# Optimization experiments

Hardware: AMD Instinct MI355X
Metric: run time of the kernel (lower is better)

## Reference

```python
import jax, jax.numpy as jnp
import numpy as np

B, NEG = 4, 33          # queries, candidates per query
N, R = 10000, 256       # entities, relation types (even; R//2 direct)
D, L = 64, 6            # hidden dim, conv layers
E, ER = 200000, 80000   # entity edges, edges per relation graph (hh/ht/th/tt)
F = 2 * D
EPS = 1e-5


def _ln(x, s, b):
    m = jnp.mean(x, -1, keepdims=True)
    v = jnp.mean((x - m) ** 2, -1, keepdims=True)
    return (x - m) * jax.lax.rsqrt(v + EPS) * s + b


def _conv(x, boundary, relation, src, dst, etype, p):
    # GeneralizedRelationalConv (dependent=False, project_relations=True):
    # distmult message, sum aggregate + boundary self-loop, update=relu(LN(Linear([x,agg])))
    p1w, p1b, p2w, p2b, lw, lb, lns, lnb = p
    rel = jax.nn.relu(relation @ p1w + p1b) @ p2w + p2b     # relation projection MLP
    msg = x[:, src, :] * rel[:, etype, :]                   # [B, Eg, D] gathered messages
    agg = jnp.zeros_like(boundary).at[:, dst, :].add(msg) + boundary
    out = jnp.concatenate([x, agg], -1) @ lw + lb
    return jax.nn.relu(_ln(out, lns, lnb))


def _entity_bf(rel_reps, h0, r0, src, dst, etype, params):
    # NBFNet Bellman-Ford over the entity graph, query-conditioned boundary
    q = rel_reps[jnp.arange(B), r0]                         # [B, D]
    boundary = jnp.zeros((B, N, D), q.dtype).at[jnp.arange(B), h0].add(q)
    x = boundary
    for i in range(L):
        x = _conv(x, boundary, rel_reps, src, dst, etype,
                  tuple(t[i] for t in params)) + x          # short_cut residual
    nq = jnp.broadcast_to(q[:, None, :], (B, N, D))
    return jnp.concatenate([x, nq], -1)                     # [B, N, 2D]


def _forward(floats, ints):
    (e1p1w, e1p1b, e1p2w, e1p2b, e1lw, e1lb, e1lns, e1lnb,
     e2p1w, e2p1b, e2p2w, e2p2b, e2lw, e2lb, e2lns, e2lnb,
     e2m1w, e2m1b, e2m2w, e2m2b,
     rp1w, rp1b, rp2w, rp2b, rlw, rlb, rlns, rlnb, nmw, nmb) = floats
    edge_src, edge_dst, edge_type, rel_src, rel_dst, rel_etype, batch = ints
    h0 = batch[:, 0, 0]
    t_idx = batch[:, :, 1]
    r0 = batch[:, 0, 2]
    e1p = (e1p1w, e1p1b, e1p2w, e1p2b, e1lw, e1lb, e1lns, e1lnb)
    # ---- RelNet over the 4 relation graphs (nodes=relations, edge types=entities) ----
    node_reps = jnp.ones((B, N, D), e1p1w.dtype)
    q = jnp.ones((B, D), e1p1w.dtype)
    boundary = jnp.zeros((B, R, D), q.dtype).at[jnp.arange(B), r0].add(q)
    x = boundary
    for i in range(L):
        h = sum(_conv(x, boundary, node_reps, rel_src[g], rel_dst[g], rel_etype[g],
                      (rp1w[g, i], rp1b[g, i], rp2w[g, i], rp2b[g, i],
                       rlw[g, i], rlb[g, i], rlns[g, i], rlnb[g, i]))
                for g in range(4))
        x = h + x                                           # short_cut
        if i == 0:
            # entity_model_1 refreshes the per-entity (relation-graph edge type) reps
            feat = _entity_bf(x, h0, r0, edge_src, edge_dst, edge_type, e1p)
            node_reps = feat @ nmw + nmb                    # [B, N, D]
    rel_reps = x                                            # [B, R, D]
    # ---- EntityNet 2: score candidates ----
    e2p = (e2p1w, e2p1b, e2p2w, e2p2b, e2lw, e2lb, e2lns, e2lnb)
    feat2 = _entity_bf(rel_reps, h0, r0, edge_src, edge_dst, edge_type, e2p)
    g = jnp.take_along_axis(feat2, jnp.broadcast_to(t_idx[:, :, None], (B, NEG, F)), axis=1)
    score = (jax.nn.relu(g @ e2m1w + e2m1b) @ e2m2w + e2m2b)[..., 0]
    return score                                            # [B, NEG]


def setup_inputs():
    key = jax.random.key(0)
    ks = iter(jax.random.split(key, 64))
    def w(shape, std=0.08):
        return jax.random.normal(next(ks), shape, jnp.float32) * std
    inp = {}
    inp["edge_src"] = jax.random.randint(next(ks), (E,), 0, N, jnp.int32)
    inp["edge_dst"] = jax.random.randint(next(ks), (E,), 0, N, jnp.int32)
    inp["edge_type"] = jax.random.randint(next(ks), (E,), 0, R, jnp.int32)
    inp["rel_src"] = jax.random.randint(next(ks), (4, ER), 0, R, jnp.int32)
    inp["rel_dst"] = jax.random.randint(next(ks), (4, ER), 0, R, jnp.int32)
    inp["rel_etype"] = jax.random.randint(next(ks), (4, ER), 0, N, jnp.int32)
    h = jax.random.randint(next(ks), (B, 1), 0, N, jnp.int32)
    t = jax.random.randint(next(ks), (B, NEG), 0, N, jnp.int32)
    r = jax.random.randint(next(ks), (B, 1), 0, R // 2, jnp.int32)
    inp["batch"] = jnp.stack([jnp.broadcast_to(h, (B, NEG)), t,
                              jnp.broadcast_to(r, (B, NEG))], -1)
    for pre in ("e1", "e2"):
        inp[pre + "p1w"] = w((L, D, D)); inp[pre + "p1b"] = jnp.zeros((L, D))
        inp[pre + "p2w"] = w((L, D, D)); inp[pre + "p2b"] = jnp.zeros((L, D))
        inp[pre + "lw"] = w((L, F, D));  inp[pre + "lb"] = jnp.zeros((L, D))
        inp[pre + "lns"] = jnp.ones((L, D)); inp[pre + "lnb"] = jnp.zeros((L, D))
    inp["e2m1w"] = w((F, F)); inp["e2m1b"] = jnp.zeros((F,))
    inp["e2m2w"] = w((F, 1)); inp["e2m2b"] = jnp.zeros((1,))
    inp["rp1w"] = w((4, L, D, D)); inp["rp1b"] = jnp.zeros((4, L, D))
    inp["rp2w"] = w((4, L, D, D)); inp["rp2b"] = jnp.zeros((4, L, D))
    inp["rlw"] = w((4, L, F, D));  inp["rlb"] = jnp.zeros((4, L, D))
    inp["rlns"] = jnp.ones((4, L, D)); inp["rlnb"] = jnp.zeros((4, L, D))
    inp["nmw"] = w((F, D)); inp["nmb"] = jnp.zeros((D,))
    return inp


def reference(e1p1w, e1p1b, e1p2w, e1p2b, e1lw, e1lb, e1lns, e1lnb,
              e2p1w, e2p1b, e2p2w, e2p2b, e2lw, e2lb, e2lns, e2lnb,
              e2m1w, e2m1b, e2m2w, e2m2b,
              rp1w, rp1b, rp2w, rp2b, rlw, rlb, rlns, rlnb, nmw, nmb,
              edge_src, edge_dst, edge_type, rel_src, rel_dst, rel_etype, batch):
    floats = (e1p1w, e1p1b, e1p2w, e1p2b, e1lw, e1lb, e1lns, e1lnb,
              e2p1w, e2p1b, e2p2w, e2p2b, e2lw, e2lb, e2lns, e2lnb,
              e2m1w, e2m1b, e2m2w, e2m2b,
              rp1w, rp1b, rp2w, rp2b, rlw, rlb, rlns, rlnb, nmw, nmb)
    ints = (edge_src, edge_dst, edge_type, rel_src, rel_dst, rel_etype, batch)
    return _forward(floats, ints)
```

## Files before the change

### kernel.cpp

```cpp
#include <hip/hip_runtime.h>

constexpr int kB   = 4;
constexpr int kNEG = 33;
constexpr int kN   = 10000;
constexpr int kR   = 256;
constexpr int kD   = 64;
constexpr int kL   = 6;
constexpr int kE   = 200000;
constexpr int kER  = 80000;

typedef const float* fp;
typedef __attribute__((ext_vector_type(8))) short bf16x8;
typedef __attribute__((ext_vector_type(4))) float f32x4;

__device__ __forceinline__ float rdlane(float v, int l) {
  return __uint_as_float(__builtin_amdgcn_readlane(__float_as_uint(v), l));
}
__device__ __forceinline__ float wave_sum64(float v) {
  #pragma unroll
  for (int o = 32; o > 0; o >>= 1) v += __shfl_xor(v, o, 64);
  return v;
}
__device__ __forceinline__ short f2bf(float x) {
  unsigned u = __float_as_uint(x);
  unsigned r = (u + 0x7fffu + ((u >> 16) & 1u)) >> 16;
  return (short)r;
}
__device__ __forceinline__ float bf2f_u(unsigned short s) {
  return __uint_as_float(((unsigned)s) << 16);
}
__device__ __forceinline__ float bf2f(short s) { return bf2f_u((unsigned short)s); }

__global__ void k_fill(float* __restrict__ p, float v, int n) {
  int i = blockIdx.x * blockDim.x + threadIdx.x;
  int stride = gridDim.x * blockDim.x;
  for (; i < n; i += stride) p[i] = v;
}
__global__ void k_zero_i(int* __restrict__ p, int n) {
  int i = blockIdx.x * blockDim.x + threadIdx.x;
  int stride = gridDim.x * blockDim.x;
  for (; i < n; i += stride) p[i] = 0;
}
__global__ void k_add_row(float* __restrict__ dst, const int* __restrict__ batch) {
  int tid = threadIdx.x;
  int b = tid >> 6, d = tid & 63;
  int row = batch[b * kNEG * 3 + 2];
  dst[((size_t)b * kR + row) * 64 + d] += 1.0f;
}
__global__ void k_get_q(float* __restrict__ q, const float* __restrict__ relx,
                        const int* __restrict__ batch) {
  int tid = threadIdx.x;
  int b = tid >> 6, d = tid & 63;
  int r0 = batch[b * kNEG * 3 + 2];
  q[b * 64 + d] = relx[((size_t)b * kR + r0) * 64 + d];
}

__global__ void k_hist(const int* __restrict__ dst, int ne, int* __restrict__ cnt) {
  int i = blockIdx.x * blockDim.x + threadIdx.x;
  if (i < ne) atomicAdd(&cnt[dst[i]], 1);
}
__global__ void k_fill_csr(const int* __restrict__ src, const int* __restrict__ dst,
                           const int* __restrict__ et, int ne,
                           int* __restrict__ cursor, int2* __restrict__ out) {
  int i = blockIdx.x * blockDim.x + threadIdx.x;
  if (i < ne) {
    int p = atomicAdd(&cursor[dst[i]], 1);
    out[p] = make_int2(src[i], et[i]);
  }
}
__global__ void k_hist_rel_lds(const int* __restrict__ rel_dst, int* __restrict__ cnt) {
  int g = blockIdx.y;
  __shared__ int lc[256];
  lc[threadIdx.x] = 0;
  __syncthreads();
  int lo = blockIdx.x * 8000, hi = min(lo + 8000, kER);
  for (int e = lo + threadIdx.x; e < hi; e += 256)
    atomicAdd(&lc[rel_dst[(size_t)g * kER + e]], 1);
  __syncthreads();
  int c = lc[threadIdx.x];
  if (c) atomicAdd(&cnt[g * 256 + threadIdx.x], c);
}
__global__ void k_fill_rel_lds(const int* __restrict__ src, const int* __restrict__ dst,
                               const int* __restrict__ et,
                               int* __restrict__ cursor, int2* __restrict__ out) {
  int g = blockIdx.y;
  __shared__ int lc[256];
  lc[threadIdx.x] = 0;
  __syncthreads();
  int lo = blockIdx.x * 8000, hi = min(lo + 8000, kER);
  const int* db = dst + (size_t)g * kER;
  for (int e = lo + threadIdx.x; e < hi; e += 256)
    atomicAdd(&lc[db[e]], 1);
  __syncthreads();
  int c = lc[threadIdx.x];
  __syncthreads();
  lc[threadIdx.x] = c ? atomicAdd(&cursor[g * 257 + threadIdx.x], c) : 0;
  __syncthreads();
  for (int e = lo + threadIdx.x; e < hi; e += 256) {
    int bin = db[e];
    int p = atomicAdd(&lc[bin], 1);
    out[(size_t)g * kER + p] = make_int2(src[(size_t)g * kER + e], et[(size_t)g * kER + e]);
  }
}
__global__ void k_scan_multi(const int* __restrict__ cnt, int* __restrict__ start,
                             int* __restrict__ cursor, int n, int cstride, int sstride) {
  const int* c = cnt + (size_t)blockIdx.x * cstride;
  int* st = start + (size_t)blockIdx.x * sstride;
  int* cu = cursor + (size_t)blockIdx.x * sstride;
  __shared__ int part[256];
  int t = threadIdx.x;
  int chunk = (n + 255) / 256;
  int lo = t * chunk, hi = min(lo + chunk, n);
  int s = 0;
  for (int i = lo; i < hi; ++i) s += c[i];
  part[t] = s;
  __syncthreads();
  if (t == 0) { int run = 0; for (int i = 0; i < 256; ++i) { int v = part[i]; part[i] = run; run += v; } }
  __syncthreads();
  int run = part[t];
  for (int i = lo; i < hi; ++i) { st[i] = run; cu[i] = run; run += c[i]; }
  if (t == 255) st[n] = run;
}

__global__ void k_packw(const float* __restrict__ w1, const float* __restrict__ w2,
                        short* __restrict__ w1h, short* __restrict__ w1l,
                        short* __restrict__ w2h, short* __restrict__ w2l) {
  int pg = blockIdx.x;
  for (int i = threadIdx.x; i < 4096; i += 256) {
    int t = i & 7, lane = (i >> 3) & 63, nt = (i >> 9) & 3, ks = i >> 11;
    int mr = lane & 15, kg = lane >> 4;
    int src = pg * 4096 + (ks * 32 + kg * 8 + t) * 64 + nt * 16 + mr;
    int dst = pg * 4096 + i;
    float v1 = w1[src]; short h1 = f2bf(v1);
    w1h[dst] = h1; w1l[dst] = f2bf(v1 - bf2f(h1));
    float v2 = w2[src]; short h2 = f2bf(v2);
    w2h[dst] = h2; w2l[dst] = f2bf(v2 - bf2f(h2));
  }
}

__global__ void __launch_bounds__(256) k_mlp_mfma(
    const float* __restrict__ in, const short* __restrict__ w1h, const short* __restrict__ w1l,
    const float* __restrict__ b1, const short* __restrict__ w2h, const short* __restrict__ w2l,
    const float* __restrict__ b2, int layer, unsigned short* __restrict__ out) {
  int g = blockIdx.y;
  int pg = g * kL + layer;
  int w = threadIdx.x >> 6, lane = threadIdx.x & 63;
  int mrow = lane & 15, kgrp = lane >> 4;
  int r0 = blockIdx.x * 64 + w * 16;
  __shared__ float hbuf[4][16][68];
  const float* xp = in + (size_t)(r0 + mrow) * 64 + kgrp * 8;
  bf16x8 a1h[2], a1l[2];
  #pragma unroll
  for (int ks = 0; ks < 2; ++ks) {
    #pragma unroll
    for (int t = 0; t < 8; ++t) {
      float v = xp[ks * 32 + t];
      short h = f2bf(v); a1h[ks][t] = h; a1l[ks][t] = f2bf(v - bf2f(h));
    }
  }
  const bf16x8* B1h = (const bf16x8*)(w1h + (size_t)pg * 4096);
  const bf16x8* B1l = (const bf16x8*)(w1l + (size_t)pg * 4096);
  #pragma unroll
  for (int nt = 0; nt < 4; ++nt) {
    f32x4 c = {0.f, 0.f, 0.f, 0.f};
    #pragma unroll
    for (int ks = 0; ks < 2; ++ks) {
      bf16x8 bh = B1h[(ks * 4 + nt) * 64 + lane];
      bf16x8 bl = B1l[(ks * 4 + nt) * 64 + lane];
      c = __builtin_amdgcn_mfma_f32_16x16x32_bf16(a1h[ks], bh, c, 0, 0, 0);
      c = __builtin_amdgcn_mfma_f32_16x16x32_bf16(a1h[ks], bl, c, 0, 0, 0);
      c = __builtin_amdgcn_mfma_f32_16x16x32_bf16(a1l[ks], bh, c, 0, 0, 0);
    }
    int col = nt * 16 + mrow;
    float bv = b1[pg * 64 + col];
    #pragma unroll
    for (int rg = 0; rg < 4; ++rg)
      hbuf[w][kgrp * 4 + rg][col] = fmaxf(c[rg] + bv, 0.f);
  }
  __syncthreads();
  bf16x8 a2h[2], a2l[2];
  #pragma unroll
  for (int ks = 0; ks < 2; ++ks) {
    #pragma unroll
    for (int t = 0; t < 8; ++t) {
      float v = hbuf[w][mrow][ks * 32 + kgrp * 8 + t];
      short h = f2bf(v); a2h[ks][t] = h; a2l[ks][t] = f2bf(v - bf2f(h));
    }
  }
  const bf16x8* B2h = (const bf16x8*)(w2h + (size_t)pg * 4096);
  const bf16x8* B2l = (const bf16x8*)(w2l + (size_t)pg * 4096);
  unsigned short* ob = out + (size_t)g * kB * kN * 64;
  #pragma unroll
  for (int nt = 0; nt < 4; ++nt) {
    f32x4 c = {0.f, 0.f, 0.f, 0.f};
    #pragma unroll
    for (int ks = 0; ks < 2; ++ks) {
      bf16x8 bh = B2h[(ks * 4 + nt) * 64 + lane];
      bf16x8 bl = B2l[(ks * 4 + nt) * 64 + lane];
      c = __builtin_amdgcn_mfma_f32_16x16x32_bf16(a2h[ks], bh, c, 0, 0, 0);
      c = __builtin_amdgcn_mfma_f32_16x16x32_bf16(a2h[ks], bl, c, 0, 0, 0);
      c = __builtin_amdgcn_mfma_f32_16x16x32_bf16(a2l[ks], bh, c, 0, 0, 0);
    }
    int col = nt * 16 + mrow;
    float bv = b2[pg * 64 + col];
    #pragma unroll
    for (int rg = 0; rg < 4; ++rg) {
      int grow = r0 + kgrp * 4 + rg;
      int bb = grow / kN;
      int nn = grow - bb * kN;
      ob[(size_t)nn * 256 + col * 4 + bb] = (unsigned short)f2bf(c[rg] + bv);
    }
  }
}

__global__ void __launch_bounds__(256) k_mlp_rel6(
    const float* __restrict__ in, fp p1w, fp p1b, fp p2w, fp p2b,
    unsigned short* __restrict__ out) {
  int j = blockIdx.y;
  int row = blockIdx.x * 4 + (threadIdx.x >> 6);
  int lane = threadIdx.x & 63;
  fp W1 = p1w + (size_t)j * 4096;
  fp W2 = p2w + (size_t)j * 4096;
  float xv = in[(size_t)row * 64 + lane];
  float a = p1b[j * 64 + lane];
  float wbuf[8];
  #pragma unroll
  for (int kk = 0; kk < 64; kk += 8) {
    #pragma unroll
    for (int u = 0; u < 8; ++u) wbuf[u] = W1[(kk + u) * 64 + lane];
    #pragma unroll
    for (int u = 0; u < 8; ++u) a = fmaf(rdlane(xv, kk + u), wbuf[u], a);
  }
  a = fmaxf(a, 0.f);
  float c = p2b[j * 64 + lane];
  #pragma unroll
  for (int kk = 0; kk < 64; kk += 8) {
    #pragma unroll
    for (int u = 0; u < 8; ++u) wbuf[u] = W2[(kk + u) * 64 + lane];
    #pragma unroll
    for (int u = 0; u < 8; ++u) c = fmaf(rdlane(a, kk + u), wbuf[u], c);
  }
  int b = row >> 8, r = row & 255;
  out[((size_t)j * kR + r) * 256 + lane * 4 + b] = (unsigned short)f2bf(c);
}

__global__ void k_gate0(fp p1w, fp p1b, fp p2w, fp p2b, float* __restrict__ gate0) {
  int g = threadIdx.x >> 6, lane = threadIdx.x & 63;
  int pg = g * kL;
  float a = p1b[pg * 64 + lane];
  #pragma unroll
  for (int k = 0; k < 64; ++k) a += p1w[(size_t)pg * 4096 + k * 64 + lane];
  a = fmaxf(a, 0.f);
  float c = p2b[pg * 64 + lane];
  #pragma unroll
  for (int k = 0; k < 64; ++k)
    c = fmaf(rdlane(a, k), p2w[(size_t)pg * 4096 + k * 64 + lane], c);
  gate0[g * 64 + lane] = c;
}
__global__ void k_rel_agg0(const int* __restrict__ rel_start, const int2* __restrict__ rel_edges,
                           const int* __restrict__ batch, const float* __restrict__ gate0,
                           float* __restrict__ agg) {
  int wid = (blockIdx.x * blockDim.x + threadIdx.x) >> 6;
  int lane = threadIdx.x & 63;
  int g = wid >> 10, rem = wid & 1023, b = rem >> 8, r = rem & 255;
  int r0 = batch[b * kNEG * 3 + 2];
  const int* start = rel_start + g * 257;
  const int2* edges = rel_edges + (size_t)g * kER;
  int s0 = start[r], s1 = start[r + 1];
  int cnt = 0;
  for (int base = s0; base < s1; base += 64) {
    int e = base + lane;
    bool m = false;
    if (e < s1) m = (edges[e].x == r0);
    cnt += (int)__popcll(__ballot(m));
  }
  agg[(size_t)wid * 64 + lane] = gate0[g * 64 + lane] * (float)cnt + ((r == r0) ? 1.f : 0.f);
}

__global__ void __launch_bounds__(256) k_gather_rel_all(
    const float* __restrict__ rxi, const unsigned short* __restrict__ gateN,
    const int* __restrict__ rel_start, const int2* __restrict__ rel_edges,
    const int* __restrict__ batch, float* __restrict__ agg) {
  int i = blockIdx.x;
  int g = i & 3, r = i >> 2;
  const unsigned short* gate = gateN + (size_t)g * kB * kN * 64;
  const int* start = rel_start + g * 257;
  const int2* edges = rel_edges + (size_t)g * kER;
  int w = threadIdx.x >> 6, lane = threadIdx.x & 63;
  int s0 = start[r], s1 = start[r + 1];
  int len = s1 - s0;
  int per = (len + 3) >> 2;
  int e0 = s0 + w * per, e1 = min(e0 + per, s1);
  float a0 = 0.f, a1 = 0.f, a2 = 0.f, a3 = 0.f;
  int2 se;
  if (e0 < e1) se = edges[e0];
  for (int e = e0; e < e1; ++e) {
    int2 cur = se;
    if (e + 1 < e1) se = edges[e + 1];
    float4 xv4 = *((const float4*)(rxi + (size_t)cur.x * 256) + lane);
    ushort4 gv4 = *((const ushort4*)(gate + (size_t)cur.y * 256) + lane);
    a0 = fmaf(xv4.x, bf2f_u(gv4.x), a0);
    a1 = fmaf(xv4.y, bf2f_u(gv4.y), a1);
    a2 = fmaf(xv4.z, bf2f_u(gv4.z), a2);
    a3 = fmaf(xv4.w, bf2f_u(gv4.w), a3);
  }
  __shared__ float red[4][4][64];
  red[w][0][lane] = a0; red[w][1][lane] = a1; red[w][2][lane] = a2; red[w][3][lane] = a3;
  __syncthreads();
  float a = red[0][w][lane] + red[1][w][lane] + red[2][w][lane] + red[3][w][lane];
  int r0b = batch[w * kNEG * 3 + 2];
  if (r == r0b) a += 1.0f;
  agg[(((size_t)g * kB + w) * kR + r) * 64 + lane] = a;
}

__global__ void __launch_bounds__(256) k_conv_rel3(
    const float* __restrict__ rel_x, float* __restrict__ agg,
    fp rlw, fp rlb, fp rlns, fp rlnb, int layer) {
  int g = blockIdx.y;
  int pg = g * kL + layer;
  int wave = threadIdx.x >> 6, lane = threadIdx.x & 63;
  int row0 = blockIdx.x * 16 + wave * 4;
  const float* xp = rel_x + (size_t)row0 * 64 + lane;
  float* ap = agg + ((size_t)g * 1024 + row0) * 64 + lane;
  float x0 = xp[0], x1 = xp[64], x2 = xp[128], x3 = xp[192];
  float g0 = ap[0], g1 = ap[64], g2 = ap[128], g3 = ap[192];
  fp w1 = rlw + (size_t)pg * 8192;
  float bv = rlb[pg * 64 + lane];
  float o0 = bv, o1 = bv, o2 = bv, o3 = bv;
  float wbuf[8];
  #pragma unroll
  for (int kk = 0; kk < 128; kk += 8) {
    #pragma unroll
    for (int u = 0; u < 8; ++u) wbuf[u] = w1[(kk + u) * 64 + lane];
    #pragma unroll
    for (int u = 0; u < 8; ++u) {
      int k = kk + u; float w = wbuf[u];
      if (k < 64) {
        o0 = fmaf(rdlane(x0, k), w, o0); o1 = fmaf(rdlane(x1, k), w, o1);
        o2 = fmaf(rdlane(x2, k), w, o2); o3 = fmaf(rdlane(x3, k), w, o3);
      } else {
        o0 = fmaf(rdlane(g0, k - 64), w, o0); o1 = fmaf(rdlane(g1, k - 64), w, o1);
        o2 = fmaf(rdlane(g2, k - 64), w, o2); o3 = fmaf(rdlane(g3, k - 64), w, o3);
      }
    }
  }
  float s = rlns[pg * 64 + lane], t = rlnb[pg * 64 + lane];
  { float m = wave_sum64(o0) * (1.f/64.f); float c = o0 - m;
    float v = wave_sum64(c*c) * (1.f/64.f);
    ap[0] = fmaxf(c * rsqrtf(v + 1e-5f) * s + t, 0.f); }
  { float m = wave_sum64(o1) * (1.f/64.f); float c = o1 - m;
    float v = wave_sum64(c*c) * (1.f/64.f);
    ap[64] = fmaxf(c * rsqrtf(v + 1e-5f) * s + t, 0.f); }
  { float m = wave_sum64(o2) * (1.f/64.f); float c = o2 - m;
    float v = wave_sum64(c*c) * (1.f/64.f);
    ap[128] = fmaxf(c * rsqrtf(v + 1e-5f) * s + t, 0.f); }
  { float m = wave_sum64(o3) * (1.f/64.f); float c = o3 - m;
    float v = wave_sum64(c*c) * (1.f/64.f);
    ap[192] = fmaxf(c * rsqrtf(v + 1e-5f) * s + t, 0.f); }
}

__global__ void k_sum_rel(float* __restrict__ rel_x, float* __restrict__ rxi,
                          const float* __restrict__ y) {
  int i = blockIdx.x * blockDim.x + threadIdx.x;
  float v = rel_x[i] + y[i] + y[65536 + i] + y[131072 + i] + y[196608 + i];
  rel_x[i] = v;
  int d = i & 63, row = i >> 6;
  int b = row >> 8, r = row & 255;
  rxi[(size_t)r * 256 + d * 4 + b] = v;
}

template<bool FIRST>
__global__ void __launch_bounds__(256) k_ent_layer2(
    const float* __restrict__ xcur, float* __restrict__ xnext,
    const unsigned short* __restrict__ xbf_cur, unsigned short* __restrict__ xbf_next,
    const unsigned short* __restrict__ gateL,
    const int* __restrict__ start, const int2* __restrict__ edges,
    const float* __restrict__ q, const int* __restrict__ batch,
    fp lw, fp lb, fp lns, fp lnb) {
  int n = (blockIdx.x * blockDim.x + threadIdx.x) >> 6;
  if (n >= kN) return;
  int lane = threadIdx.x & 63;
  int h0[4]; float qv[4];
  #pragma unroll
  for (int b = 0; b < 4; ++b) { h0[b] = batch[b * kNEG * 3]; qv[b] = q[b * 64 + lane]; }
  float a0 = 0.f, a1 = 0.f, a2 = 0.f, a3 = 0.f;
  int s0 = start[n], s1 = start[n + 1];
  int2 se;
  if (s0 < s1) se = edges[s0];
  for (int e = s0; e < s1; ++e) {
    int2 cur = se;
    if (e + 1 < s1) se = edges[e + 1];
    ushort4 gv4 = *((const ushort4*)(gateL + (size_t)cur.y * 256) + lane);
    if (FIRST) {
      if (cur.x == h0[0]) a0 = fmaf(qv[0], bf2f_u(gv4.x), a0);
      if (cur.x == h0[1]) a1 = fmaf(qv[1], bf2f_u(gv4.y), a1);
      if (cur.x == h0[2]) a2 = fmaf(qv[2], bf2f_u(gv4.z), a2);
      if (cur.x == h0[3]) a3 = fmaf(qv[3], bf2f_u(gv4.w), a3);
    } else {
      ushort4 xv4 = *((const ushort4*)(xbf_cur + (size_t)cur.x * 256) + lane);
      a0 = fmaf(bf2f_u(xv4.x), bf2f_u(gv4.x), a0);
      a1 = fmaf(bf2f_u(xv4.y), bf2f_u(gv4.y), a1);
      a2 = fmaf(bf2f_u(xv4.z), bf2f_u(gv4.z), a2);
      a3 = fmaf(bf2f_u(xv4.w), bf2f_u(gv4.w), a3);
    }
  }
  if (n == h0[0]) a0 += qv[0];
  if (n == h0[1]) a1 += qv[1];
  if (n == h0[2]) a2 += qv[2];
  if (n == h0[3]) a3 += qv[3];
  float x0, x1, x2, x3;
  if (FIRST) {
    x0 = (n == h0[0]) ? qv[0] : 0.f; x1 = (n == h0[1]) ? qv[1] : 0.f;
    x2 = (n == h0[2]) ? qv[2] : 0.f; x3 = (n == h0[3]) ? qv[3] : 0.f;
  } else {
    const float* xp = xcur + (size_t)n * 64 + lane;
    x0 = xp[0]; x1 = xp[640000]; x2 = xp[1280000]; x3 = xp[1920000];
  }
  float bv = lb[lane];
  float o0 = bv, o1 = bv, o2 = bv, o3 = bv;
  float wbuf[8];
  #pragma unroll
  for (int kk = 0; kk < 128; kk += 8) {
    #pragma unroll
    for (int u = 0; u < 8; ++u) wbuf[u] = lw[(kk + u) * 64 + lane];
    #pragma unroll
    for (int u = 0; u < 8; ++u) {
      int k = kk + u; float w = wbuf[u];
      if (k < 64) {
        o0 = fmaf(rdlane(x0, k), w, o0); o1 = fmaf(rdlane(x1, k), w, o1);
        o2 = fmaf(rdlane(x2, k), w, o2); o3 = fmaf(rdlane(x3, k), w, o3);
      } else {
        o0 = fmaf(rdlane(a0, k - 64), w, o0); o1 = fmaf(rdlane(a1, k - 64), w, o1);
        o2 = fmaf(rdlane(a2, k - 64), w, o2); o3 = fmaf(rdlane(a3, k - 64), w, o3);
      }
    }
  }
  float s = lns[lane], t = lnb[lane];
  float* yp = xnext + (size_t)n * 64 + lane;
  float y0, y1, y2, y3;
  { float m = wave_sum64(o0) * (1.f/64.f); float c = o0 - m;
    float v = wave_sum64(c*c) * (1.f/64.f);
    y0 = x0 + fmaxf(c * rsqrtf(v + 1e-5f) * s + t, 0.f); yp[0] = y0; }
  { float m = wave_sum64(o1) * (1.f/64.f); float c = o1 - m;
    float v = wave_sum64(c*c) * (1.f/64.f);
    y1 = x1 + fmaxf(c * rsqrtf(v + 1e-5f) * s + t, 0.f); yp[640000] = y1; }
  { float m = wave_sum64(o2) * (1.f/64.f); float c = o2 - m;
    float v = wave_sum64(c*c) * (1.f/64.f);
    y2 = x2 + fmaxf(c * rsqrtf(v + 1e-5f) * s + t, 0.f); yp[1280000] = y2; }
  { float m = wave_sum64(o3) * (1.f/64.f); float c = o3 - m;
    float v = wave_sum64(c*c) * (1.f/64.f);
    y3 = x3 + fmaxf(c * rsqrtf(v + 1e-5f) * s + t, 0.f); yp[1920000] = y3; }
  ushort4 m4;
  m4.x = (unsigned short)f2bf(y0); m4.y = (unsigned short)f2bf(y1);
  m4.z = (unsigned short)f2bf(y2); m4.w = (unsigned short)f2bf(y3);
  *((ushort4*)(xbf_next + (size_t)n * 256) + lane) = m4;
}

__global__ void __launch_bounds__(256) k_nodeup4(
    const float* __restrict__ x, const float* __restrict__ q,
    fp nmw, fp nmb, float* __restrict__ out) {
  int wid = (blockIdx.x * blockDim.x + threadIdx.x) >> 6;
  int lane = threadIdx.x & 63;
  int r0 = wid * 4;
  if (r0 >= kB * kN) return;
  int b = r0 / kN;
  const float* ip = x + (size_t)r0 * 64 + lane;
  float x0 = ip[0], x1 = ip[64], x2 = ip[128], x3 = ip[192];
  float qv = q[b * 64 + lane];
  float bv = nmb[lane];
  float c0 = bv, c1 = bv, c2 = bv, c3 = bv;
  float wbuf[4];
  #pragma unroll
  for (int kk = 0; kk < 64; kk += 4) {
    #pragma unroll
    for (int u = 0; u < 4; ++u) wbuf[u] = nmw[(kk + u) * 64 + lane];
    #pragma unroll
    for (int u = 0; u < 4; ++u) {
      int k = kk + u; float w = wbuf[u];
      c0 = fmaf(rdlane(x0, k), w, c0); c1 = fmaf(rdlane(x1, k), w, c1);
      c2 = fmaf(rdlane(x2, k), w, c2); c3 = fmaf(rdlane(x3, k), w, c3);
    }
  }
  float qa = 0.f;
  #pragma unroll
  for (int k = 0; k < 64; ++k)
    qa = fmaf(rdlane(qv, k), nmw[(64 + k) * 64 + lane], qa);
  float* op = out + (size_t)r0 * 64 + lane;
  op[0] = c0 + qa; op[64] = c1 + qa; op[128] = c2 + qa; op[192] = c3 + qa;
}

__global__ void k_score(const float* __restrict__ entx, const float* __restrict__ q,
                        const int* __restrict__ batch,
                        fp m1w, fp m1b, fp m2w, fp m2b,
                        float* __restrict__ out) {
  int b = blockIdx.x / kNEG, n = blockIdx.x % kNEG;
  int t = batch[(b * kNEG + n) * 3 + 1];
  int j = threadIdx.x;
  __shared__ float gv[128];
  __shared__ float red[2];
  gv[j] = (j < 64) ? entx[((size_t)b * kN + t) * 64 + j] : q[b * 64 + (j - 64)];
  __syncthreads();
  float acc = m1b[j];
  #pragma unroll 16
  for (int k = 0; k < 128; ++k)
    acc = fmaf(gv[k], m1w[k * 128 + j], acc);
  float h = fmaxf(acc, 0.f) * m2w[j];
  h = wave_sum64(h);
  if ((j & 63) == 0) red[j >> 6] = h;
  __syncthreads();
  if (j == 0) out[b * kNEG + n] = red[0] + red[1] + m2b[0];
}

extern "C" void kernel_launch(void* const* d_in, const int* in_sizes, int n_in,
                              void* d_out, int out_size, void* d_ws, size_t ws_size,
                              hipStream_t stream) {
  const int* edge_src  = (const int*)d_in[0];
  const int* edge_dst  = (const int*)d_in[1];
  const int* edge_type = (const int*)d_in[2];
  const int* rel_src   = (const int*)d_in[3];
  const int* rel_dst   = (const int*)d_in[4];
  const int* rel_etype = (const int*)d_in[5];
  const int* batch     = (const int*)d_in[6];
  fp e1p1w = (fp)d_in[7],  e1p1b = (fp)d_in[8],  e1p2w = (fp)d_in[9],  e1p2b = (fp)d_in[10];
  fp e1lw  = (fp)d_in[11], e1lb  = (fp)d_in[12], e1lns = (fp)d_in[13], e1lnb = (fp)d_in[14];
  fp e2p1w = (fp)d_in[15], e2p1b = (fp)d_in[16], e2p2w = (fp)d_in[17], e2p2b = (fp)d_in[18];
  fp e2lw  = (fp)d_in[19], e2lb  = (fp)d_in[20], e2lns = (fp)d_in[21], e2lnb = (fp)d_in[22];
  fp e2m1w = (fp)d_in[23], e2m1b = (fp)d_in[24], e2m2w = (fp)d_in[25], e2m2b = (fp)d_in[26];
  fp rp1w  = (fp)d_in[27], rp1b  = (fp)d_in[28], rp2w  = (fp)d_in[29], rp2b  = (fp)d_in[30];
  fp rlw   = (fp)d_in[31], rlb   = (fp)d_in[32], rlns  = (fp)d_in[33], rlnb  = (fp)d_in[34];
  fp nmw   = (fp)d_in[35], nmb   = (fp)d_in[36];

  float* ws = (float*)d_ws;
  float* rel_x     = ws;
  float* q         = rel_x + 65536;
  float* gate0     = q + 256;
  float* rxi       = gate0 + 256;
  float* rel_agg   = rxi + 65536;
  float* node_reps = rel_agg + 262144;
  float* ent_xa    = node_reps + 2560000;
  float* ent_xb    = ent_xa + 2560000;
  unsigned short* gateR6 = (unsigned short*)(ent_xb + 2560000);
  unsigned short* gateN  = gateR6 + 393216;
  unsigned short* ent_ba = gateN + 10240000;
  unsigned short* ent_bb = ent_ba + 2560000;
  int*   iws       = (int*)(ent_bb + 2560000);
  int2*  ent_edges = (int2*)iws;
  int2*  rel_edges = (int2*)(iws + 400000);
  int*   ent_cnt   = iws + 400000 + 640000;
  int*   ent_start = ent_cnt + 10000;
  int*   ent_cur   = ent_start + 10001;
  int*   rel_cnt   = ent_cur + 10001;
  int*   rel_start = rel_cnt + 1024;
  int*   rel_cur   = rel_start + 1028;
  short* w1hp      = (short*)(rel_cur + 1028 + 2);
  short* w1lp      = w1hp + 98304;
  short* w2hp      = w1lp + 98304;
  short* w2lp      = w2hp + 98304;

  const int nZero = 10000 + 10001 + 10001 + 1024;
  k_zero_i<<<(nZero + 255) / 256, 256, 0, stream>>>(ent_cnt, nZero);
  k_hist<<<(kE + 255) / 256, 256, 0, stream>>>(edge_dst, kE, ent_cnt);
  k_hist_rel_lds<<<dim3(10, 4), 256, 0, stream>>>(rel_dst, rel_cnt);
  k_scan_multi<<<1, 256, 0, stream>>>(ent_cnt, ent_start, ent_cur, 10000, 0, 0);
  k_scan_multi<<<4, 256, 0, stream>>>(rel_cnt, rel_start, rel_cur, 256, 256, 257);
  k_fill_csr<<<(kE + 255) / 256, 256, 0, stream>>>(edge_src, edge_dst, edge_type, kE, ent_cur, ent_edges);
  k_fill_rel_lds<<<dim3(10, 4), 256, 0, stream>>>(rel_src, rel_dst, rel_etype, rel_cur, rel_edges);
  k_packw<<<24, 256, 0, stream>>>(rp1w, rp2w, w1hp, w1lp, w2hp, w2lp);

  k_fill<<<256, 256, 0, stream>>>(rel_x, 0.f, kB * kR * kD);
  k_add_row<<<1, 256, 0, stream>>>(rel_x, batch);

  k_gate0<<<1, 256, 0, stream>>>(rp1w, rp1b, rp2w, rp2b, gate0);
  k_rel_agg0<<<1024, 256, 0, stream>>>(rel_start, rel_edges, batch, gate0, rel_agg);
  k_conv_rel3<<<dim3(64, 4), 256, 0, stream>>>(rel_x, rel_agg, rlw, rlb, rlns, rlnb, 0);
  k_sum_rel<<<256, 256, 0, stream>>>(rel_x, rxi, rel_agg);

  k_get_q<<<1, 256, 0, stream>>>(q, rel_x, batch);
  k_mlp_rel6<<<dim3(256, 6), 256, 0, stream>>>(rel_x, e1p1w, e1p1b, e1p2w, e1p2b, gateR6);
  {
    float* cur = ent_xa; float* nxt = ent_xb;
    unsigned short* bcur = ent_ba; unsigned short* bnxt = ent_bb;
    for (int j = 0; j < kL; ++j) {
      const unsigned short* gL = gateR6 + (size_t)j * kR * 256;
      if (j == 0)
        k_ent_layer2<true><<<2500, 256, 0, stream>>>(cur, nxt, bcur, bnxt, gL, ent_start, ent_edges, q, batch,
            e1lw + (size_t)j * 8192, e1lb + (size_t)j * 64, e1lns + (size_t)j * 64, e1lnb + (size_t)j * 64);
      else
        k_ent_layer2<false><<<2500, 256, 0, stream>>>(cur, nxt, bcur, bnxt, gL, ent_start, ent_edges, q, batch,
            e1lw + (size_t)j * 8192, e1lb + (size_t)j * 64, e1lns + (size_t)j * 64, e1lnb + (size_t)j * 64);
      float* tf = cur; cur = nxt; nxt = tf;
      unsigned short* tb = bcur; bcur = bnxt; bnxt = tb;
    }
    k_nodeup4<<<2500, 256, 0, stream>>>(cur, q, nmw, nmb, node_reps);
  }

  for (int i = 1; i < kL; ++i) {
    k_mlp_mfma<<<dim3(625, 4), 256, 0, stream>>>(node_reps, w1hp, w1lp, rp1b, w2hp, w2lp, rp2b, i, gateN);
    k_gather_rel_all<<<1024, 256, 0, stream>>>(rxi, gateN, rel_start, rel_edges, batch, rel_agg);
    k_conv_rel3<<<dim3(64, 4), 256, 0, stream>>>(rel_x, rel_agg, rlw, rlb, rlns, rlnb, i);
    k_sum_rel<<<256, 256, 0, stream>>>(rel_x, rxi, rel_agg);
  }

  k_get_q<<<1, 256, 0, stream>>>(q, rel_x, batch);
  k_mlp_rel6<<<dim3(256, 6), 256, 0, stream>>>(rel_x, e2p1w, e2p1b, e2p2w, e2p2b, gateR6);
  {
    float* cur = ent_xa; float* nxt = ent_xb;
    unsigned short* bcur = ent_ba; unsigned short* bnxt = ent_bb;
    for (int j = 0; j < kL; ++j) {
      const unsigned short* gL = gateR6 + (size_t)j * kR * 256;
      if (j == 0)
        k_ent_layer2<true><<<2500, 256, 0, stream>>>(cur, nxt, bcur, bnxt, gL, ent_start, ent_edges, q, batch,
            e2lw + (size_t)j * 8192, e2lb + (size_t)j * 64, e2lns + (size_t)j * 64, e2lnb + (size_t)j * 64);
      else
        k_ent_layer2<false><<<2500, 256, 0, stream>>>(cur, nxt, bcur, bnxt, gL, ent_start, ent_edges, q, batch,
            e2lw + (size_t)j * 8192, e2lb + (size_t)j * 64, e2lns + (size_t)j * 64, e2lnb + (size_t)j * 64);
      float* tf = cur; cur = nxt; nxt = tf;
      unsigned short* tb = bcur; bcur = bnxt; bnxt = tb;
    }
    k_score<<<kB * kNEG, 128, 0, stream>>>(cur, q, batch, e2m1w, e2m1b, e2m2w, e2m2b, (float*)d_out);
  }
}
```

Before: 1.011 ms.

## Split entity layer into gather kernel and split-bf16 MFMA linear+LayerNorm kernel

The fused entity conv kernel is split in two. One kernel does the edge gather and writes the aggregate to a new fp32 buffer. The second does the [x,agg]·W linear with bf16 MFMA using a hi/lo split to keep near-fp32 accuracy, then LayerNorm, ReLU and the residual. This replaces the per-wave readlane/FMA scalar GEMM with matrix cores, at the cost of an extra round trip for the aggregate, extra launches, and an explicit zero-fill of the initial x buffer.

```diff
diff --git a/kernel.cpp b/kernel.cpp
--- a/kernel.cpp
+++ b/kernel.cpp
@@ -21,6 +21,11 @@
   for (int o = 32; o > 0; o >>= 1) v += __shfl_xor(v, o, 64);
   return v;
 }
+__device__ __forceinline__ float group_sum16(float v) {
+  #pragma unroll
+  for (int o = 8; o > 0; o >>= 1) v += __shfl_xor(v, o, 64);
+  return v;
+}
 __device__ __forceinline__ short f2bf(float x) {
   unsigned u = __float_as_uint(x);
   unsigned r = (u + 0x7fffu + ((u >> 16) & 1u)) >> 16;
@@ -46,6 +51,13 @@
   int b = tid >> 6, d = tid & 63;
   int row = batch[b * kNEG * 3 + 2];
   dst[((size_t)b * kR + row) * 64 + d] += 1.0f;
+}
+__global__ void k_add_row_ent(float* __restrict__ dst, const int* __restrict__ batch,
+                              const float* __restrict__ q) {
+  int tid = threadIdx.x;
+  int b = tid >> 6, d = tid & 63;
+  int row = batch[b * kNEG * 3];
+  dst[((size_t)b * kN + row) * 64 + d] += q[b * 64 + d];
 }
 __global__ void k_get_q(float* __restrict__ q, const float* __restrict__ relx,
                         const int* __restrict__ batch) {
@@ -135,6 +147,17 @@
     w1h[dst] = h1; w1l[dst] = f2bf(v1 - bf2f(h1));
     float v2 = w2[src]; short h2 = f2bf(v2);
     w2h[dst] = h2; w2l[dst] = f2bf(v2 - bf2f(h2));
+  }
+}
+__global__ void k_packw_e(const float* __restrict__ w, short* __restrict__ wh, short* __restrict__ wl) {
+  int set = blockIdx.x;
+  for (int i = threadIdx.x; i < 8192; i += 256) {
+    int t = i & 7, lane = (i >> 3) & 63, nt = (i >> 9) & 3, ks = i >> 11;
+    int mr = lane & 15, kg = lane >> 4;
+    int src = set * 8192 + (ks * 32 + kg * 8 + t) * 64 + nt * 16 + mr;
+    int dst = set * 8192 + i;
+    float v = w[src]; short h = f2bf(v);
+    wh[dst] = h; wl[dst] = f2bf(v - bf2f(h));
   }
 }
 
@@ -370,13 +393,11 @@
 }
 
 template<bool FIRST>
-__global__ void __launch_bounds__(256) k_ent_layer2(
-    const float* __restrict__ xcur, float* __restrict__ xnext,
-    const unsigned short* __restrict__ xbf_cur, unsigned short* __restrict__ xbf_next,
-    const unsigned short* __restrict__ gateL,
+__global__ void __launch_bounds__(256) k_ent_gather(
+    const unsigned short* __restrict__ xbf_cur, const unsigned short* __restrict__ gateL,
     const int* __restrict__ start, const int2* __restrict__ edges,
     const float* __restrict__ q, const int* __restrict__ batch,
-    fp lw, fp lb, fp lns, fp lnb) {
+    float* __restrict__ agg) {
   int n = (blockIdx.x * blockDim.x + threadIdx.x) >> 6;
   if (n >= kN) return;
   int lane = threadIdx.x & 63;
@@ -408,52 +429,73 @@
   if (n == h0[1]) a1 += qv[1];
   if (n == h0[2]) a2 += qv[2];
   if (n == h0[3]) a3 += qv[3];
-  float x0, x1, x2, x3;
-  if (FIRST) {
-    x0 = (n == h0[0]) ? qv[0] : 0.f; x1 = (n == h0[1]) ? qv[1] : 0.f;
-    x2 = (n == h0[2]) ? qv[2] : 0.f; x3 = (n == h0[3]) ? qv[3] : 0.f;
-  } else {
-    const float* xp = xcur + (size_t)n * 64 + lane;
-    x0 = xp[0]; x1 = xp[640000]; x2 = xp[1280000]; x3 = xp[1920000];
-  }
-  float bv = lb[lane];
-  float o0 = bv, o1 = bv, o2 = bv, o3 = bv;
-  float wbuf[8];
-  #pragma unroll
-  for (int kk = 0; kk < 128; kk += 8) {
-    #pragma unroll
-    for (int u = 0; u < 8; ++u) wbuf[u] = lw[(kk + u) * 64 + lane];
-    #pragma unroll
-    for (int u = 0; u < 8; ++u) {
-      int k = kk + u; float w = wbuf[u];
-      if (k < 64) {
-        o0 = fmaf(rdlane(x0, k), w, o0); o1 = fmaf(rdlane(x1, k), w, o1);
-        o2 = fmaf(rdlane(x2, k), w, o2); o3 = fmaf(rdlane(x3, k), w, o3);
-      } else {
-        o0 = fmaf(rdlane(a0, k - 64), w, o0); o1 = fmaf(rdlane(a1, k - 64), w, o1);
-        o2 = fmaf(rdlane(a2, k - 64), w, o2); o3 = fmaf(rdlane(a3, k - 64), w, o3);
-      }
-    }
-  }
-  float s = lns[lane], t = lnb[lane];
-  float* yp = xnext + (size_t)n * 64 + lane;
-  float y0, y1, y2, y3;
-  { float m = wave_sum64(o0) * (1.f/64.f); float c = o0 - m;
-    float v = wave_sum64(c*c) * (1.f/64.f);
-    y0 = x0 + fmaxf(c * rsqrtf(v + 1e-5f) * s + t, 0.f); yp[0] = y0; }
-  { float m = wave_sum64(o1) * (1.f/64.f); float c = o1 - m;
-    float v = wave_sum64(c*c) * (1.f/64.f);
-    y1 = x1 + fmaxf(c * rsqrtf(v + 1e-5f) * s + t, 0.f); yp[640000] = y1; }
-  { float m = wave_sum64(o2) * (1.f/64.f); float c = o2 - m;
-    float v = wave_sum64(c*c) * (1.f/64.f);
-    y2 = x2 + fmaxf(c * rsqrtf(v + 1e-5f) * s + t, 0.f); yp[1280000] = y2; }
-  { float m = wave_sum64(o3) * (1.f/64.f); float c = o3 - m;
-    float v = wave_sum64(c*c) * (1.f/64.f);
-    y3 = x3 + fmaxf(c * rsqrtf(v + 1e-5f) * s + t, 0.f); yp[1920000] = y3; }
-  ushort4 m4;
-  m4.x = (unsigned short)f2bf(y0); m4.y = (unsigned short)f2bf(y1);
-  m4.z = (unsigned short)f2bf(y2); m4.w = (unsigned short)f2bf(y3);
-  *((ushort4*)(xbf_next + (size_t)n * 256) + lane) = m4;
+  float* ap = agg + (size_t)n * 64 + lane;
+  ap[0] = a0; ap[640000] = a1; ap[1280000] = a2; ap[1920000] = a3;
+}
+
+__global__ void __launch_bounds__(256) k_ent_conv_mfma(
+    const float* __restrict__ xcur, const float* __restrict__ aggv,
+    float* __restrict__ xnext, unsigned short* __restrict__ xbf_next,
+    const short* __restrict__ wh, const short* __restrict__ wl, int set,
+    fp lb, fp lns, fp lnb) {
+  int w = threadIdx.x >> 6, lane = threadIdx.x & 63;
+  int mrow = lane & 15, kgrp = lane >> 4;
+  int r0 = blockIdx.x * 64 + w * 16;
+  int arow = r0 + mrow;
+  bf16x8 ah[4], al[4];
+  #pragma unroll
+  for (int ks = 0; ks < 4; ++ks) {
+    const float* p = (ks < 2) ? (xcur + (size_t)arow * 64 + ks * 32 + kgrp * 8)
+                              : (aggv + (size_t)arow * 64 + (ks - 2) * 32 + kgrp * 8);
+    #pragma unroll
+    for (int t = 0; t < 8; ++t) {
+      float v = p[t];
+      short h = f2bf(v); ah[ks][t] = h; al[ks][t] = f2bf(v - bf2f(h));
+    }
+  }
+  const bf16x8* Bh = (const bf16x8*)(wh + (size_t)set * 8192);
+  const bf16x8* Bl = (const bf16x8*)(wl + (size_t)set * 8192);
+  float o[4][4];
+  #pragma unroll
+  for (int nt = 0; nt < 4; ++nt) {
+    f32x4 c = {0.f, 0.f, 0.f, 0.f};
+    #pragma unroll
+    for (int ks = 0; ks < 4; ++ks) {
+      bf16x8 bh = Bh[(ks * 4 + nt) * 64 + lane];
+      bf16x8 bl = Bl[(ks * 4 + nt) * 64 + lane];
+      c = __builtin_amdgcn_mfma_f32_16x16x32_bf16(ah[ks], bh, c, 0, 0, 0);
+      c = __builtin_amdgcn_mfma_f32_16x16x32_bf16(ah[ks], bl, c, 0, 0, 0);
+      c = __builtin_amdgcn_mfma_f32_16x16x32_bf16(al[ks], bh, c, 0, 0, 0);
+    }
+    float bv = lb[nt * 16 + mrow];
+    #pragma unroll
+    for (int rg = 0; rg < 4; ++rg) o[nt][rg] = c[rg] + bv;
+  }
+  float mean[4], varr[4];
+  #pragma unroll
+  for (int rg = 0; rg < 4; ++rg) {
+    float p = o[0][rg] + o[1][rg] + o[2][rg] + o[3][rg];
+    mean[rg] = group_sum16(p) * (1.f / 64.f);
+    float d0 = o[0][rg] - mean[rg], d1 = o[1][rg] - mean[rg];
+    float d2 = o[2][rg] - mean[rg], d3 = o[3][rg] - mean[rg];
+    float vs = d0 * d0 + d1 * d1 + d2 * d2 + d3 * d3;
+    varr[rg] = group_sum16(vs) * (1.f / 64.f);
+  }
+  #pragma unroll
+  for (int nt = 0; nt < 4; ++nt) {
+    int col = nt * 16 + mrow;
+    float s = lns[col], tt = lnb[col];
+    #pragma unroll
+    for (int rg = 0; rg < 4; ++rg) {
+      int grow = r0 + kgrp * 4 + rg;
+      float xv = xcur[(size_t)grow * 64 + col];
+      float y = xv + fmaxf((o[nt][rg] - mean[rg]) * rsqrtf(varr[rg] + 1e-5f) * s + tt, 0.f);
+      xnext[(size_t)grow * 64 + col] = y;
+      int bb = grow / kN;
+      int nn = grow - bb * kN;
+      xbf_next[(size_t)nn * 256 + col * 4 + bb] = (unsigned short)f2bf(y);
+    }
+  }
 }
 
 __global__ void __launch_bounds__(256) k_nodeup4(
@@ -539,7 +581,8 @@
   float* node_reps = rel_agg + 262144;
   float* ent_xa    = node_reps + 2560000;
   float* ent_xb    = ent_xa + 2560000;
-  unsigned short* gateR6 = (unsigned short*)(ent_xb + 2560000);
+  float* ent_agg   = ent_xb + 2560000;
+  unsigned short* gateR6 = (unsigned short*)(ent_agg + 2560000);
   unsigned short* gateN  = gateR6 + 393216;
   unsigned short* ent_ba = gateN + 10240000;
   unsigned short* ent_bb = ent_ba + 2560000;
@@ -556,6 +599,8 @@
   short* w1lp      = w1hp + 98304;
   short* w2hp      = w1lp + 98304;
   short* w2lp      = w2hp + 98304;
+  short* elwh      = w2lp + 98304;
+  short* elwl      = elwh + 98304;
 
   const int nZero = 10000 + 10001 + 10001 + 1024;
   k_zero_i<<<(nZero + 255) / 256, 256, 0, stream>>>(ent_cnt, nZero);
@@ -566,6 +611,8 @@
   k_fill_csr<<<(kE + 255) / 256, 256, 0, stream>>>(edge_src, edge_dst, edge_type, kE, ent_cur, ent_edges);
   k_fill_rel_lds<<<dim3(10, 4), 256, 0, stream>>>(rel_src, rel_dst, rel_etype, rel_cur, rel_edges);
   k_packw<<<24, 256, 0, stream>>>(rp1w, rp2w, w1hp, w1lp, w2hp, w2lp);
+  k_packw_e<<<6, 256, 0, stream>>>(e1lw, elwh, elwl);
+  k_packw_e<<<6, 256, 0, stream>>>(e2lw, elwh + 6 * 8192, elwl + 6 * 8192);
 
   k_fill<<<256, 256, 0, stream>>>(rel_x, 0.f, kB * kR * kD);
   k_add_row<<<1, 256, 0, stream>>>(rel_x, batch);
@@ -577,17 +624,19 @@
 
   k_get_q<<<1, 256, 0, stream>>>(q, rel_x, batch);
   k_mlp_rel6<<<dim3(256, 6), 256, 0, stream>>>(rel_x, e1p1w, e1p1b, e1p2w, e1p2b, gateR6);
+  k_fill<<<2048, 256, 0, stream>>>(ent_xa, 0.f, kB * kN * kD);
+  k_add_row_ent<<<1, 256, 0, stream>>>(ent_xa, batch, q);
   {
     float* cur = ent_xa; float* nxt = ent_xb;
     unsigned short* bcur = ent_ba; unsigned short* bnxt = ent_bb;
     for (int j = 0; j < kL; ++j) {
       const unsigned short* gL = gateR6 + (size_t)j * kR * 256;
       if (j == 0)
-        k_ent_layer2<true><<<2500, 256, 0, stream>>>(cur, nxt, bcur, bnxt, gL, ent_start, ent_edges, q, batch,
-            e1lw + (size_t)j * 8192, e1lb + (size_t)j * 64, e1lns + (size_t)j * 64, e1lnb + (size_t)j * 64);
+        k_ent_gather<true><<<2500, 256, 0, stream>>>(bcur, gL, ent_start, ent_edges, q, batch, ent_agg);
       else
-        k_ent_layer2<false><<<2500, 256, 0, stream>>>(cur, nxt, bcur, bnxt, gL, ent_start, ent_edges, q, batch,
-            e1lw + (size_t)j * 8192, e1lb + (size_t)j * 64, e1lns + (size_t)j * 64, e1lnb + (size_t)j * 64);
+        k_ent_gather<false><<<2500, 256, 0, stream>>>(bcur, gL, ent_start, ent_edges, q, batch, ent_agg);
+      k_ent_conv_mfma<<<625, 256, 0, stream>>>(cur, ent_agg, nxt, bnxt, elwh, elwl, j,
+          e1lb + (size_t)j * 64, e1lns + (size_t)j * 64, e1lnb + (size_t)j * 64);
       float* tf = cur; cur = nxt; nxt = tf;
       unsigned short* tb = bcur; bcur = bnxt; bnxt = tb;
     }
@@ -603,17 +652,19 @@
 
   k_get_q<<<1, 256, 0, stream>>>(q, rel_x, batch);
   k_mlp_rel6<<<dim3(256, 6), 256, 0, stream>>>(rel_x, e2p1w, e2p1b, e2p2w, e2p2b, gateR6);
+  k_fill<<<2048, 256, 0, stream>>>(ent_xa, 0.f, kB * kN * kD);
+  k_add_row_ent<<<1, 256, 0, stream>>>(ent_xa, batch, q);
   {
     float* cur = ent_xa; float* nxt = ent_xb;
     unsigned short* bcur = ent_ba; unsigned short* bnxt = ent_bb;
     for (int j = 0; j < kL; ++j) {
       const unsigned short* gL = gateR6 + (size_t)j * kR * 256;
       if (j == 0)
-        k_ent_layer2<true><<<2500, 256, 0, stream>>>(cur, nxt, bcur, bnxt, gL, ent_start, ent_edges, q, batch,
-            e2lw + (size_t)j * 8192, e2lb + (size_t)j * 64, e2lns + (size_t)j * 64, e2lnb + (size_t)j * 64);
+        k_ent_gather<true><<<2500, 256, 0, stream>>>(bcur, gL, ent_start, ent_edges, q, batch, ent_agg);
       else
-        k_ent_layer2<false><<<2500, 256, 0, stream>>>(cur, nxt, bcur, bnxt, gL, ent_start, ent_edges, q, batch,
-            e2lw + (size_t)j * 8192, e2lb + (size_t)j * 64, e2lns + (size_t)j * 64, e2lnb + (size_t)j * 64);
+        k_ent_gather<false><<<2500, 256, 0, stream>>>(bcur, gL, ent_start, ent_edges, q, batch, ent_agg);
+      k_ent_conv_mfma<<<625, 256, 0, stream>>>(cur, ent_agg, nxt, bnxt, elwh, elwl, 6 + j,
+          e2lb + (size_t)j * 64, e2lns + (size_t)j * 64, e2lnb + (size_t)j * 64);
       float* tf = cur; cur = nxt; nxt = tf;
       unsigned short* tb = bcur; bcur = bnxt; bnxt = tb;
     }
```

New measurement: 1.002 ms (median of 2 runs). About the same (-0.8%).
